# Performance work log

Measured on AMD Instinct MI355X. Metric: run time of the kernel, lower is better.

Reference implementation:

```python
import jax, jax.numpy as jnp
import numpy as np

N_WIN = 7    # n_win hardcoded in AR_Attention
TOPK = 4     # topk routing windows
HEADS = 8    # num_heads


def setup_inputs() -> dict:
    key = jax.random.key(0)
    ks = jax.random.split(key, 6)
    B, H, W, C = 4, 56, 56, 256
    s = 0.02
    x = jax.random.normal(ks[0], (B, H, W, C), jnp.float32)
    Wqkv = jax.random.normal(ks[1], (C, 3 * C), jnp.float32) * s  # Linear(dim, 3*dim) (qk_dim=dim)
    bqkv = jnp.zeros((3 * C,), jnp.float32)
    Wo = jax.random.normal(ks[2], (C, C), jnp.float32) * s        # output projection Linear(dim, dim)
    bo = jnp.zeros((C,), jnp.float32)
    lepe_w = jax.random.normal(ks[3], (5, 5, 1, C), jnp.float32) * s  # 5x5 depthwise conv (side_dwconv=5)
    lepe_b = jnp.zeros((C,), jnp.float32)
    return {"x": x, "Wqkv": Wqkv, "bqkv": bqkv, "Wo": Wo, "bo": bo,
            "lepe_w": lepe_w, "lepe_b": lepe_b}


def reference(x, Wqkv, bqkv, Wo, bo, lepe_w, lepe_b):
    B, H, W, C = x.shape
    nw = N_WIN
    h, w = H // nw, W // nw           # region size (8x8)
    p2 = nw * nw                      # number of regions (49)
    hd = C // HEADS                   # head dim
    scale = float(C) ** -0.5          # qk_scale = qk_dim ** -0.5 (qk_dim = dim)

    # region partition: [B,H,W,C] -> [B,p2,h,w,C]
    xr = x.reshape(B, nw, h, nw, w, C).transpose(0, 1, 3, 2, 4, 5).reshape(B, p2, h, w, C)

    qkv = xr @ Wqkv + bqkv            # [B,p2,h,w,3C]
    q, kv = qkv[..., :C], qkv[..., C:]

    q_pix = q.reshape(B, p2, h * w, C)
    kv_pix = kv.reshape(B, p2, h * w, 2 * C)   # kv_downsample_mode='identity'

    # region-level queries/keys via per-window mean pooling
    q_win = q.mean((2, 3))                     # [B,p2,C]
    k_win = kv[..., :C].mean((2, 3))           # [B,p2,C]

    # LEPE: 5x5 depthwise conv on v over the full image grid
    v_img = kv[..., C:].reshape(B, nw, nw, h, w, C).transpose(0, 1, 3, 2, 4, 5).reshape(B, H, W, C)
    lepe = jax.lax.conv_general_dilated(
        v_img, lepe_w, (1, 1), 'SAME',
        dimension_numbers=('NHWC', 'HWIO', 'NHWC'),
        feature_group_count=C) + lepe_b

    # top-k window routing (param_routing=False, hard routing, mul_weight='none')
    r_logit = jnp.einsum('bpc,bqc->bpq', q_win * scale, k_win)  # [B,p2,p2]
    _, r_idx = jax.lax.top_k(r_logit, TOPK)                     # [B,p2,TOPK]

    # gather selected kv windows: [B,p2,TOPK,h*w,2C]
    kv_sel = jax.vmap(lambda kvp, i: kvp[i])(kv_pix, r_idx)

    k_sel = kv_sel[..., :C].reshape(B, p2, TOPK * h * w, HEADS, hd)
    v_sel = kv_sel[..., C:].reshape(B, p2, TOPK * h * w, HEADS, hd)
    qh = q_pix.reshape(B, p2, h * w, HEADS, hd)

    attn = jnp.einsum('bpqnd,bpknd->bpnqk', qh * scale, k_sel)  # [B,p2,heads,hw,TOPK*hw]
    attn = jax.nn.softmax(attn, axis=-1)
    out = jnp.einsum('bpnqk,bpknd->bpqnd', attn, v_sel).reshape(B, p2, h, w, C)

    # windows back to image grid
    out = out.reshape(B, nw, nw, h, w, C).transpose(0, 1, 3, 2, 4, 5).reshape(B, H, W, C)
    out = out + lepe
    return out @ Wo + bo
```

## Files before the change

kernel.cpp:

```cpp
#include <hip/hip_runtime.h>
#include <hip/hip_bf16.h>

#define NPIX 12544

typedef short bf16x8 __attribute__((ext_vector_type(8)));
typedef short bf16x4 __attribute__((ext_vector_type(4)));
typedef float f32x4  __attribute__((ext_vector_type(4)));

__device__ __forceinline__ float bf2f(unsigned short u) {
    unsigned int x = ((unsigned int)u) << 16;
    float f; __builtin_memcpy(&f, &x, sizeof(f)); return f;
}
__device__ __forceinline__ unsigned short f2bf(float f) {
    __hip_bfloat16 h = __float2bfloat16(f);
    unsigned short u; __builtin_memcpy(&u, &h, 2); return u;
}
__device__ __forceinline__ void load_lds16(const unsigned short* g, unsigned short* l) {
    __builtin_amdgcn_global_load_lds(
        (const __attribute__((address_space(1))) unsigned int*)g,
        (__attribute__((address_space(3))) unsigned int*)l,
        16, 0, 0);
}
__device__ __forceinline__ unsigned ldsoff(const void* p) {
    return (unsigned)(unsigned long long)(const __attribute__((address_space(3))) char*)p;
}
template<int OFF>
__device__ __forceinline__ bf16x4 tr16(unsigned addr) {
    bf16x4 d;
    asm volatile("ds_read_b64_tr_b16 %0, %1 offset:%c2"
                 : "=v"(d) : "v"(addr), "i"(OFF));
    return d;
}

__global__ __launch_bounds__(256) void k_prep(
    const float* __restrict__ X, unsigned short* __restrict__ Xb,
    float* __restrict__ xmean,
    const float* __restrict__ Wqkv, const float* __restrict__ Wo,
    unsigned short* __restrict__ Wtq, unsigned short* __restrict__ Wto)
{
    __shared__ __align__(16) unsigned char sm[64 * 65 * 4];
    const int t = threadIdx.x;
    const int blk = blockIdx.x;
    if (blk < 392) {
        float* part = (float*)sm;
        const int w = blk >> 1, hc = blk & 1;
        const int b = w / 49, p = w % 49;
        const int wi = p / 7, wj = p % 7;
        const int ch0 = hc * 128;
        const int ps = t >> 5, cg = t & 31;
        float4 s = {0.f, 0.f, 0.f, 0.f};
        #pragma unroll
        for (int i = 0; i < 8; i++) {
            int pp = ps * 8 + i;
            int y = wi * 8 + (pp >> 3), x = wj * 8 + (pp & 7);
            int idx = (((b * 56) + y) * 56 + x) * 256 + ch0 + cg * 4;
            float4 v = *reinterpret_cast<const float4*>(X + idx);
            s.x += v.x; s.y += v.y; s.z += v.z; s.w += v.w;
            ushort4 o = { f2bf(v.x), f2bf(v.y), f2bf(v.z), f2bf(v.w) };
            *reinterpret_cast<ushort4*>(Xb + idx) = o;
        }
        *reinterpret_cast<float4*>(part + t * 4) = *reinterpret_cast<float4*>(&s);
        __syncthreads();
        if (t < 32) {
            float4 m = {0.f, 0.f, 0.f, 0.f};
            #pragma unroll
            for (int ps2 = 0; ps2 < 8; ps2++) {
                float4 v = *reinterpret_cast<float4*>(part + (ps2 * 32 + t) * 4);
                m.x += v.x; m.y += v.y; m.z += v.z; m.w += v.w;
            }
            m.x *= (1.f / 64.f); m.y *= (1.f / 64.f);
            m.z *= (1.f / 64.f); m.w *= (1.f / 64.f);
            *reinterpret_cast<float4*>(xmean + w * 256 + ch0 + t * 4) = m;
        }
    } else {
        float* tile = (float*)sm;
        int tb = blk - 392;
        const float* Wsrc; unsigned short* Wdst; int N, kt, nt;
        if (tb < 48) { Wsrc = Wqkv; Wdst = Wtq; N = 768; kt = tb / 12; nt = tb % 12; }
        else { tb -= 48; Wsrc = Wo; Wdst = Wto; N = 256; kt = tb / 4; nt = tb % 4; }
        const int k0 = kt * 64, n0 = nt * 64;
        const int r0 = t >> 6, c = t & 63;
        #pragma unroll
        for (int i = 0; i < 16; i++) {
            int r = i * 4 + r0;
            tile[r * 65 + c] = Wsrc[(size_t)(k0 + r) * N + n0 + c];
        }
        __syncthreads();
        #pragma unroll
        for (int i = 0; i < 16; i++) {
            int n = i * 4 + r0;
            Wdst[(size_t)(n0 + n) * 256 + k0 + c] = f2bf(tile[c * 65 + n]);
        }
    }
}

__global__ __launch_bounds__(256) void k_main1(
    const unsigned short* __restrict__ A,
    const unsigned short* __restrict__ Bt,
    const float* __restrict__ bias,
    unsigned short* __restrict__ O,
    const float* __restrict__ xmean,
    const float* __restrict__ Wqkv,
    float* __restrict__ qwin, float* __restrict__ kwin)
{
    __shared__ __align__(16) unsigned char sm1[32768];
    const int t = threadIdx.x;
    const int blk = blockIdx.x;
    if (blk < 588) {
        unsigned short* As = (unsigned short*)sm1;
        unsigned short* Bs = (unsigned short*)(sm1 + 16384);
        const int m0 = (blk % 98) * 128, n0 = (blk / 98) * 128;
        const int wave = t >> 6, lane = t & 63, quad = lane >> 4, lo = lane & 15;
        const int wm = wave & 1, wn = wave >> 1;
        const int sr = wave * 16 + (lane >> 2);
        const int sc = lane & 3;
        f32x4 acc[4][4];
        #pragma unroll
        for (int i = 0; i < 4; i++)
            #pragma unroll
            for (int j = 0; j < 4; j++) acc[i][j] = (f32x4){0.f, 0.f, 0.f, 0.f};

        auto stage = [&](int it) {
            int kt = it * 32;
            unsigned short* Ad = As + (it & 1) * 4096;
            unsigned short* Bd = Bs + (it & 1) * 4096;
            #pragma unroll
            for (int j = 0; j < 2; j++) {
                int row = j * 64 + sr;
                int e = sc ^ ((row >> 1) & 3);
                load_lds16(A  + (size_t)(m0 + row) * 256 + kt + e * 8, &Ad[row * 32 + sc * 8]);
                load_lds16(Bt + (size_t)(n0 + row) * 256 + kt + e * 8, &Bd[row * 32 + sc * 8]);
            }
        };
        stage(0);
        for (int it = 0; it < 8; ++it) {
            if (it < 7) {
                stage(it + 1);
                asm volatile("s_waitcnt vmcnt(4)" ::: "memory");
            } else {
                asm volatile("s_waitcnt vmcnt(0)" ::: "memory");
            }
            __builtin_amdgcn_s_barrier();
            const unsigned short* Ac = As + (it & 1) * 4096;
            const unsigned short* Bc = Bs + (it & 1) * 4096;
            bf16x8 af[4], bfr[4];
            #pragma unroll
            for (int mt = 0; mt < 4; mt++) {
                int row = wm * 64 + mt * 16 + lo;
                int c = quad ^ ((row >> 1) & 3);
                af[mt] = *reinterpret_cast<const bf16x8*>(&Ac[row * 32 + c * 8]);
            }
            #pragma unroll
            for (int nt = 0; nt < 4; nt++) {
                int col = wn * 64 + nt * 16 + lo;
                int c = quad ^ ((col >> 1) & 3);
                bfr[nt] = *reinterpret_cast<const bf16x8*>(&Bc[col * 32 + c * 8]);
            }
            #pragma unroll
            for (int mt = 0; mt < 4; mt++)
                #pragma unroll
                for (int nt = 0; nt < 4; nt++)
                    acc[mt][nt] = __builtin_amdgcn_mfma_f32_16x16x32_bf16(
                        af[mt], bfr[nt], acc[mt][nt], 0, 0, 0);
            __builtin_amdgcn_s_barrier();
        }
        float bv[4];
        #pragma unroll
        for (int nt = 0; nt < 4; nt++) bv[nt] = bias[n0 + wn * 64 + nt * 16 + lo];
        #pragma unroll
        for (int mt = 0; mt < 4; mt++)
            #pragma unroll
            for (int nt = 0; nt < 4; nt++) {
                int n = n0 + wn * 64 + nt * 16 + lo;
                #pragma unroll
                for (int r = 0; r < 4; r++) {
                    int m = m0 + wm * 64 + mt * 16 + quad * 4 + r;
                    O[m * 768 + n] = f2bf(acc[mt][nt][r] + bv[nt]);
                }
            }
    } else {
        float* xs = (float*)sm1;
        const int u = blk - 588;
        const int bp = u % 196;
        const int half = u / 196;
        const int c = t;
        xs[c] = xmean[bp * 256 + c];
        __syncthreads();
        const int col = half * 256 + c;
        float a = 0.f;
        for (int k = 0; k < 256; k++) a += xs[k] * Wqkv[k * 768 + col];
        float* outp = half ? kwin : qwin;
        outp[bp * 256 + c] = a + bias[col];
    }
}

__global__ __launch_bounds__(256) void k_main2(
    const float* __restrict__ qwin, const float* __restrict__ kwin,
    int* __restrict__ ridx)
{
    __shared__ __align__(16) unsigned char sm2[1024];
    const int t = threadIdx.x;
    const int blk = blockIdx.x;
    float* part = (float*)sm2;
    float* lg   = (float*)(sm2 + 49 * 4 * 4);
    const int b = blk / 49, p = blk % 49;
    if (t < 196) {
        int d = t >> 2, pr = t & 3;
        const float* qp = &qwin[(b * 49 + p) * 256];
        const float* kp = &kwin[(b * 49 + d) * 256];
        float a = 0.f;
        for (int ch = pr * 64; ch < pr * 64 + 64; ch++) a += qp[ch] * kp[ch];
        part[d * 4 + pr] = a;
    }
    __syncthreads();
    if (t < 49) lg[t] = part[t * 4 + 0] + part[t * 4 + 1] + part[t * 4 + 2] + part[t * 4 + 3];
    __syncthreads();
    if (t == 0) {
        unsigned long long used = 0ull;
        for (int sel = 0; sel < 4; sel++) {
            float best = -1e30f; int bi = 0;
            for (int qq = 0; qq < 49; qq++)
                if (!((used >> qq) & 1ull) && lg[qq] > best) { best = lg[qq]; bi = qq; }
            used |= (1ull << bi);
            ridx[blk * 4 + sel] = bi;
        }
    }
}

__global__ __launch_bounds__(256) void k_attn(
    const unsigned short* __restrict__ QKV,
    const int* __restrict__ ridx,
    const float* __restrict__ lw, const float* __restrict__ lb,
    unsigned short* __restrict__ Osum)
{
    __shared__ __align__(16) unsigned char smem[40064];
    unsigned short* Vs  = (unsigned short*)smem;
    unsigned short* Ks  = (unsigned short*)(smem + 16384);
    unsigned short* PST = (unsigned short*)(smem + 32768);
    float* lws          = (float*)(smem + 36864);

    const int p = blockIdx.x, head = blockIdx.y, b = blockIdx.z;
    const int t = threadIdx.x;
    const int wi = p / 7, wj = p % 7;
    const int wave = t >> 6, lane = t & 63, quad = lane >> 4, lo = lane & 15;
    const int pix4 = t >> 2, c4 = t & 3;

    const int q  = wave * 16 + lo;
    const int qy = wi * 8 + (q >> 3), qx = wj * 8 + (q & 7);

    bf16x8 af = *reinterpret_cast<const bf16x8*>(
        QKV + (size_t)(((b * 56) + qy) * 56 + qx) * 768 + head * 32 + quad * 8);

    if (t < 200) {
        int tap = t >> 3, ci = (t & 7) * 4;
        *reinterpret_cast<float4*>(&lws[tap * 32 + ci]) =
            *reinterpret_cast<const float4*>(lw + tap * 256 + head * 32 + ci);
    }
    {
        const int4 rs = *reinterpret_cast<const int4*>(&ridx[(b * 49 + p) * 4]);
        const int sels[4] = { rs.x, rs.y, rs.z, rs.w };
        #pragma unroll
        for (int pass = 0; pass < 4; pass++) {
            int sel = sels[pass];
            int si = sel / 7, sj = sel % 7;
            int y = si * 8 + (pix4 >> 3), x = sj * 8 + (pix4 & 7);
            const unsigned short* base = QKV + (((b * 56) + y) * 56 + x) * 768 + 256 + head * 32;
            bf16x8 kv = *reinterpret_cast<const bf16x8*>(base + c4 * 8);
            bf16x8 vv = *reinterpret_cast<const bf16x8*>(base + 256 + c4 * 8);
            int krow = pass * 64 + pix4;
            *reinterpret_cast<bf16x8*>(&Ks[krow * 32 + c4 * 8]) = kv;
            *reinterpret_cast<bf16x8*>(
                &Vs[(krow >> 2) * 128 + (c4 >> 1) * 64 + (krow & 3) * 16 + (c4 & 1) * 8]) = vv;
        }
    }
    __syncthreads();

    float lep[8];
    {
        float4 b0 = *reinterpret_cast<const float4*>(lb + head * 32 + quad * 8);
        float4 b1 = *reinterpret_cast<const float4*>(lb + head * 32 + quad * 8 + 4);
        lep[0] = b0.x; lep[1] = b0.y; lep[2] = b0.z; lep[3] = b0.w;
        lep[4] = b1.x; lep[5] = b1.y; lep[6] = b1.z; lep[7] = b1.w;
        #pragma unroll
        for (int ky = 0; ky < 5; ky++) {
            int yy = qy + ky - 2;
            int yc = min(max(yy, 0), 55);
            bool yin = (yy >= 0) & (yy < 56);
            #pragma unroll
            for (int kx = 0; kx < 5; kx++) {
                int xx = qx + kx - 2;
                int xc = min(max(xx, 0), 55);
                float mf = (yin & (xx >= 0) & (xx < 56)) ? 1.f : 0.f;
                bf16x8 v = *reinterpret_cast<const bf16x8*>(
                    QKV + (size_t)(((b * 56) + yc) * 56 + xc) * 768 + 512 + head * 32 + quad * 8);
                const float* wrow = &lws[(ky * 5 + kx) * 32 + quad * 8];
                float4 w0 = *reinterpret_cast<const float4*>(wrow);
                float4 w1 = *reinterpret_cast<const float4*>(wrow + 4);
                lep[0] += bf2f((unsigned short)v[0]) * w0.x * mf;
                lep[1] += bf2f((unsigned short)v[1]) * w0.y * mf;
                lep[2] += bf2f((unsigned short)v[2]) * w0.z * mf;
                lep[3] += bf2f((unsigned short)v[3]) * w0.w * mf;
                lep[4] += bf2f((unsigned short)v[4]) * w1.x * mf;
                lep[5] += bf2f((unsigned short)v[5]) * w1.y * mf;
                lep[6] += bf2f((unsigned short)v[6]) * w1.z * mf;
                lep[7] += bf2f((unsigned short)v[7]) * w1.w * mf;
            }
        }
    }

    const f32x4 z = (f32x4){0.f, 0.f, 0.f, 0.f};

    float M[4] = {-1e30f, -1e30f, -1e30f, -1e30f};
    #pragma unroll 4
    for (int nt = 0; nt < 16; nt++) {
        bf16x8 bfr = *reinterpret_cast<const bf16x8*>(&Ks[(nt * 16 + lo) * 32 + quad * 8]);
        f32x4 s = __builtin_amdgcn_mfma_f32_16x16x32_bf16(af, bfr, z, 0, 0, 0);
        #pragma unroll
        for (int r = 0; r < 4; r++) M[r] = fmaxf(M[r], s[r] * 0.0625f);
    }
    #pragma unroll
    for (int d = 1; d < 16; d <<= 1)
        #pragma unroll
        for (int r = 0; r < 4; r++) M[r] = fmaxf(M[r], __shfl_xor(M[r], d));

    unsigned short* myP = PST + wave * 512;
    const unsigned pbase = ldsoff(myP) + quad * 256 + lo * 8;
    const unsigned vbase = ldsoff(Vs)  + quad * 512 + lo * 8;
    float l[4] = {0.f, 0.f, 0.f, 0.f};
    f32x4 o0 = z, o1 = z;
    for (int c = 0; c < 8; c++) {
        bf16x8 k0 = *reinterpret_cast<const bf16x8*>(&Ks[((2 * c) * 16 + lo) * 32 + quad * 8]);
        bf16x8 k1 = *reinterpret_cast<const bf16x8*>(&Ks[((2 * c + 1) * 16 + lo) * 32 + quad * 8]);
        f32x4 s0 = __builtin_amdgcn_mfma_f32_16x16x32_bf16(af, k0, z, 0, 0, 0);
        f32x4 s1 = __builtin_amdgcn_mfma_f32_16x16x32_bf16(af, k1, z, 0, 0, 0);
        float e0[4], e1[4];
        #pragma unroll
        for (int r = 0; r < 4; r++) {
            e0[r] = __expf(s0[r] * 0.0625f - M[r]);
            e1[r] = __expf(s1[r] * 0.0625f - M[r]);
            l[r] += e0[r] + e1[r];
        }
        ushort4 p0 = { f2bf(e0[0]), f2bf(e0[1]), f2bf(e0[2]), f2bf(e0[3]) };
        ushort4 p1 = { f2bf(e1[0]), f2bf(e1[1]), f2bf(e1[2]), f2bf(e1[3]) };
        *reinterpret_cast<ushort4*>(&myP[lo * 16 + quad * 4]) = p0;
        *reinterpret_cast<ushort4*>(&myP[(16 + lo) * 16 + quad * 4]) = p1;
        asm volatile("s_waitcnt lgkmcnt(0)" ::: "memory");
        __builtin_amdgcn_sched_barrier(0);

        const unsigned vb = vbase + c * 2048;
        bf16x4 ra0  = tr16<0>(pbase);
        bf16x4 ra1  = tr16<128>(pbase);
        bf16x4 rw00 = tr16<0>(vb);
        bf16x4 rw01 = tr16<256>(vb);
        bf16x4 rw10 = tr16<128>(vb);
        bf16x4 rw11 = tr16<384>(vb);
        asm volatile("s_waitcnt lgkmcnt(0)" ::: "memory");
        __builtin_amdgcn_sched_barrier(0);
        bf16x8 pa, vb0, vb1;
        #pragma unroll
        for (int j = 0; j < 4; j++) {
            pa[j]  = ra0[j];  pa[4 + j]  = ra1[j];
            vb0[j] = rw00[j]; vb0[4 + j] = rw01[j];
            vb1[j] = rw10[j]; vb1[4 + j] = rw11[j];
        }
        o0 = __builtin_amdgcn_mfma_f32_16x16x32_bf16(pa, vb0, o0, 0, 0, 0);
        o1 = __builtin_amdgcn_mfma_f32_16x16x32_bf16(pa, vb1, o1, 0, 0, 0);
    }
    #pragma unroll
    for (int d = 1; d < 16; d <<= 1)
        #pragma unroll
        for (int r = 0; r < 4; r++) l[r] += __shfl_xor(l[r], d);

    {
        float i0 = 1.f / l[0], i1 = 1.f / l[1], i2 = 1.f / l[2], i3 = 1.f / l[3];
        ushort4 p0 = { f2bf(o0[0] * i0), f2bf(o0[1] * i1),
                       f2bf(o0[2] * i2), f2bf(o0[3] * i3) };
        ushort4 p1 = { f2bf(o1[0] * i0), f2bf(o1[1] * i1),
                       f2bf(o1[2] * i2), f2bf(o1[3] * i3) };
        *reinterpret_cast<ushort4*>(&myP[lo * 16 + quad * 4]) = p0;
        *reinterpret_cast<ushort4*>(&myP[(16 + lo) * 16 + quad * 4]) = p1;
    }
    const unsigned oaddr = ldsoff(myP) + quad * 256 + lo * 8;
    asm volatile("s_waitcnt lgkmcnt(0)" ::: "memory");
    __builtin_amdgcn_sched_barrier(0);
    bf16x4 e0 = tr16<0>(oaddr);
    bf16x4 e1 = tr16<128>(oaddr);
    asm volatile("s_waitcnt lgkmcnt(0)" ::: "memory");
    __builtin_amdgcn_sched_barrier(0);
    {
        size_t gbase = (size_t)(((b * 56) + qy) * 56 + qx) * 256 + head * 32 + quad * 8;
        bf16x8 oo;
        #pragma unroll
        for (int j = 0; j < 4; j++) {
            oo[j]     = (short)f2bf(bf2f((unsigned short)e0[j]) + lep[j]);
            oo[4 + j] = (short)f2bf(bf2f((unsigned short)e1[j]) + lep[4 + j]);
        }
        *reinterpret_cast<bf16x8*>(Osum + gbase) = oo;
    }
}

__global__ __launch_bounds__(256) void k_proj(
    const unsigned short* __restrict__ A,
    const unsigned short* __restrict__ Bt,
    const float* __restrict__ bias,
    float* __restrict__ O)
{
    __shared__ __align__(16) unsigned short As[2 * 128 * 32];
    __shared__ __align__(16) unsigned short Bs[2 * 64 * 32];
    const int t = threadIdx.x;
    const int m0 = blockIdx.x * 128, n0 = blockIdx.y * 64;
    const int wave = t >> 6, lane = t & 63, quad = lane >> 4, lo = lane & 15;
    const int sr = wave * 16 + (lane >> 2);
    const int sc = lane & 3;
    f32x4 acc[2][4];
    #pragma unroll
    for (int i = 0; i < 2; i++)
        #pragma unroll
        for (int j = 0; j < 4; j++) acc[i][j] = (f32x4){0.f, 0.f, 0.f, 0.f};

    auto stage = [&](int it) {
        int kt = it * 32;
        unsigned short* Ad = As + (it & 1) * 4096;
        unsigned short* Bd = Bs + (it & 1) * 2048;
        #pragma unroll
        for (int j = 0; j < 2; j++) {
            int row = j * 64 + sr;
            int e = sc ^ ((row >> 1) & 3);
            load_lds16(A + (size_t)(m0 + row) * 256 + kt + e * 8, &Ad[row * 32 + sc * 8]);
        }
        {
            int e = sc ^ ((sr >> 1) & 3);
            load_lds16(Bt + (size_t)(n0 + sr) * 256 + kt + e * 8, &Bd[sr * 32 + sc * 8]);
        }
    };
    stage(0);
    for (int it = 0; it < 8; ++it) {
        if (it < 7) {
            stage(it + 1);
            asm volatile("s_waitcnt vmcnt(3)" ::: "memory");
        } else {
            asm volatile("s_waitcnt vmcnt(0)" ::: "memory");
        }
        __builtin_amdgcn_s_barrier();
        const unsigned short* Ac = As + (it & 1) * 4096;
        const unsigned short* Bc = Bs + (it & 1) * 2048;
        bf16x8 af[2], bfr[4];
        #pragma unroll
        for (int mt = 0; mt < 2; mt++) {
            int row = wave * 32 + mt * 16 + lo;
            int c = quad ^ ((row >> 1) & 3);
            af[mt] = *reinterpret_cast<const bf16x8*>(&Ac[row * 32 + c * 8]);
        }
        #pragma unroll
        for (int nt = 0; nt < 4; nt++) {
            int col = nt * 16 + lo;
            int c = quad ^ ((col >> 1) & 3);
            bfr[nt] = *reinterpret_cast<const bf16x8*>(&Bc[col * 32 + c * 8]);
        }
        #pragma unroll
        for (int mt = 0; mt < 2; mt++)
            #pragma unroll
            for (int nt = 0; nt < 4; nt++)
                acc[mt][nt] = __builtin_amdgcn_mfma_f32_16x16x32_bf16(
                    af[mt], bfr[nt], acc[mt][nt], 0, 0, 0);
        __builtin_amdgcn_s_barrier();
    }
    float bv[4];
    #pragma unroll
    for (int nt = 0; nt < 4; nt++) bv[nt] = bias[n0 + nt * 16 + lo];
    #pragma unroll
    for (int mt = 0; mt < 2; mt++)
        #pragma unroll
        for (int nt = 0; nt < 4; nt++) {
            int n = n0 + nt * 16 + lo;
            #pragma unroll
            for (int r = 0; r < 4; r++) {
                int m = m0 + wave * 32 + mt * 16 + quad * 4 + r;
                O[m * 256 + n] = acc[mt][nt][r] + bv[nt];
            }
        }
}

extern "C" void kernel_launch(void* const* d_in, const int* in_sizes, int n_in,
                              void* d_out, int out_size, void* d_ws, size_t ws_size,
                              hipStream_t stream)
{
    const float* x    = (const float*)d_in[0];
    const float* Wqkv = (const float*)d_in[1];
    const float* bqkv = (const float*)d_in[2];
    const float* Wo   = (const float*)d_in[3];
    const float* bo   = (const float*)d_in[4];
    const float* lw   = (const float*)d_in[5];
    const float* lb   = (const float*)d_in[6];
    float* out = (float*)d_out;

    char* ws = (char*)d_ws;
    size_t off = 0;
    unsigned short* qkv   = (unsigned short*)(ws + off); off += (size_t)NPIX * 768 * 2;
    unsigned short* xb    = (unsigned short*)(ws + off); off += (size_t)NPIX * 256 * 2;
    unsigned short* Wtq   = (unsigned short*)(ws + off); off += 768 * 256 * 2;
    unsigned short* Wto   = (unsigned short*)(ws + off); off += 256 * 256 * 2;
    unsigned short* Osum  = (unsigned short*)(ws + off); off += (size_t)NPIX * 256 * 2;
    float* xmean = (float*)(ws + off); off += 196 * 256 * 4;
    float* qwin  = (float*)(ws + off); off += 196 * 256 * 4;
    float* kwin  = (float*)(ws + off); off += 196 * 256 * 4;
    int*   ridx  = (int*)(ws + off);   off += 196 * 4 * 4;

    k_prep <<<dim3(456),      256, 0, stream>>>(x, xb, xmean, Wqkv, Wo, Wtq, Wto);
    k_main1<<<dim3(980),      256, 0, stream>>>(xb, Wtq, bqkv, qkv, xmean, Wqkv, qwin, kwin);
    k_main2<<<dim3(196),      256, 0, stream>>>(qwin, kwin, ridx);
    k_attn <<<dim3(49, 8, 4), 256, 0, stream>>>(qkv, ridx, lw, lb, Osum);
    k_proj <<<dim3(98, 4),    256, 0, stream>>>(Osum, Wto, bo, out);
}
```

Baseline: 181.2 us.

## Move LEPE depthwise conv out of attention into routing kernel as separate blocks

The 5x5 depthwise LEPE conv is taken out of the attention kernel and computed by extra blocks appended to the routing kernel. Those blocks write a bf16 LEPE buffer, and the attention kernel reads it back at the end. This is meant to shorten the attention kernel's critical path and register and LDS use, and to run the conv alongside the small routing work. The cost is an extra global write and read of a pixel-by-channel bf16 buffer, plus one more rounding of the LEPE term to bf16.

```diff
diff --git a/kernel.cpp b/kernel.cpp
--- a/kernel.cpp
+++ b/kernel.cpp
@@ -196,48 +196,99 @@
 
 __global__ __launch_bounds__(256) void k_main2(
     const float* __restrict__ qwin, const float* __restrict__ kwin,
-    int* __restrict__ ridx)
+    int* __restrict__ ridx,
+    const unsigned short* __restrict__ QKV,
+    const float* __restrict__ lw, const float* __restrict__ lb,
+    unsigned short* __restrict__ Olepe)
 {
-    __shared__ __align__(16) unsigned char sm2[1024];
+    __shared__ __align__(16) unsigned char sm2[25600];
     const int t = threadIdx.x;
     const int blk = blockIdx.x;
-    float* part = (float*)sm2;
-    float* lg   = (float*)(sm2 + 49 * 4 * 4);
-    const int b = blk / 49, p = blk % 49;
-    if (t < 196) {
-        int d = t >> 2, pr = t & 3;
-        const float* qp = &qwin[(b * 49 + p) * 256];
-        const float* kp = &kwin[(b * 49 + d) * 256];
-        float a = 0.f;
-        for (int ch = pr * 64; ch < pr * 64 + 64; ch++) a += qp[ch] * kp[ch];
-        part[d * 4 + pr] = a;
-    }
-    __syncthreads();
-    if (t < 49) lg[t] = part[t * 4 + 0] + part[t * 4 + 1] + part[t * 4 + 2] + part[t * 4 + 3];
-    __syncthreads();
-    if (t == 0) {
-        unsigned long long used = 0ull;
-        for (int sel = 0; sel < 4; sel++) {
-            float best = -1e30f; int bi = 0;
-            for (int qq = 0; qq < 49; qq++)
-                if (!((used >> qq) & 1ull) && lg[qq] > best) { best = lg[qq]; bi = qq; }
-            used |= (1ull << bi);
-            ridx[blk * 4 + sel] = bi;
-        }
+    if (blk < 196) {
+        float* part = (float*)sm2;
+        float* lg   = (float*)(sm2 + 49 * 4 * 4);
+        const int b = blk / 49, p = blk % 49;
+        if (t < 196) {
+            int d = t >> 2, pr = t & 3;
+            const float* qp = &qwin[(b * 49 + p) * 256];
+            const float* kp = &kwin[(b * 49 + d) * 256];
+            float a = 0.f;
+            for (int ch = pr * 64; ch < pr * 64 + 64; ch++) a += qp[ch] * kp[ch];
+            part[d * 4 + pr] = a;
+        }
+        __syncthreads();
+        if (t < 49) lg[t] = part[t * 4 + 0] + part[t * 4 + 1] + part[t * 4 + 2] + part[t * 4 + 3];
+        __syncthreads();
+        if (t == 0) {
+            unsigned long long used = 0ull;
+            for (int sel = 0; sel < 4; sel++) {
+                float best = -1e30f; int bi = 0;
+                for (int qq = 0; qq < 49; qq++)
+                    if (!((used >> qq) & 1ull) && lg[qq] > best) { best = lg[qq]; bi = qq; }
+                used |= (1ull << bi);
+                ridx[blk * 4 + sel] = bi;
+            }
+        }
+    } else {
+        float* lws = (float*)sm2;
+        #pragma unroll
+        for (int i = 0; i < 25; i++) lws[i * 256 + t] = lw[i * 256 + t];
+
+        const int pl = t & 7;
+        const int cg = t >> 3;
+        const int c0 = cg * 8;
+        const int gid = (blk - 196) * 8 + pl;
+        const int b = gid / 3136, rem = gid % 3136;
+        const int y = rem / 56, x = rem % 56;
+        __syncthreads();
+
+        float acc[8];
+        {
+            float4 b0 = *reinterpret_cast<const float4*>(lb + c0);
+            float4 b1 = *reinterpret_cast<const float4*>(lb + c0 + 4);
+            acc[0] = b0.x; acc[1] = b0.y; acc[2] = b0.z; acc[3] = b0.w;
+            acc[4] = b1.x; acc[5] = b1.y; acc[6] = b1.z; acc[7] = b1.w;
+        }
+        #pragma unroll
+        for (int ky = 0; ky < 5; ky++) {
+            int yy = y + ky - 2;
+            if (yy < 0 || yy >= 56) continue;
+            #pragma unroll
+            for (int kx = 0; kx < 5; kx++) {
+                int xx = x + kx - 2;
+                if (xx < 0 || xx >= 56) continue;
+                bf16x8 v = *reinterpret_cast<const bf16x8*>(
+                    QKV + (((b * 56) + yy) * 56 + xx) * 768 + 512 + c0);
+                const float* wrow = &lws[(ky * 5 + kx) * 256 + c0];
+                float4 w0 = *reinterpret_cast<const float4*>(wrow);
+                float4 w1 = *reinterpret_cast<const float4*>(wrow + 4);
+                acc[0] += bf2f((unsigned short)v[0]) * w0.x;
+                acc[1] += bf2f((unsigned short)v[1]) * w0.y;
+                acc[2] += bf2f((unsigned short)v[2]) * w0.z;
+                acc[3] += bf2f((unsigned short)v[3]) * w0.w;
+                acc[4] += bf2f((unsigned short)v[4]) * w1.x;
+                acc[5] += bf2f((unsigned short)v[5]) * w1.y;
+                acc[6] += bf2f((unsigned short)v[6]) * w1.z;
+                acc[7] += bf2f((unsigned short)v[7]) * w1.w;
+            }
+        }
+        bf16x8 o;
+        #pragma unroll
+        for (int j = 0; j < 8; j++) o[j] = (short)f2bf(acc[j]);
+        *reinterpret_cast<bf16x8*>(Olepe + (size_t)gid * 256 + c0) = o;
     }
 }
 
 __global__ __launch_bounds__(256) void k_attn(
     const unsigned short* __restrict__ QKV,
     const int* __restrict__ ridx,
-    const float* __restrict__ lw, const float* __restrict__ lb,
+    const unsigned short* __restrict__ Olepe,
     unsigned short* __restrict__ Osum)
 {
-    __shared__ __align__(16) unsigned char smem[40064];
+    __shared__ __align__(16) unsigned char smem[36864];
     unsigned short* Vs  = (unsigned short*)smem;
     unsigned short* Ks  = (unsigned short*)(smem + 16384);
     unsigned short* PST = (unsigned short*)(smem + 32768);
-    float* lws          = (float*)(smem + 36864);
 
     const int p = blockIdx.x, head = blockIdx.y, b = blockIdx.z;
     const int t = threadIdx.x;
@@ -251,11 +302,6 @@
     bf16x8 af = *reinterpret_cast<const bf16x8*>(
         QKV + (size_t)(((b * 56) + qy) * 56 + qx) * 768 + head * 32 + quad * 8);
 
-    if (t < 200) {
-        int tap = t >> 3, ci = (t & 7) * 4;
-        *reinterpret_cast<float4*>(&lws[tap * 32 + ci]) =
-            *reinterpret_cast<const float4*>(lw + tap * 256 + head * 32 + ci);
-    }
     {
         const int4 rs = *reinterpret_cast<const int4*>(&ridx[(b * 49 + p) * 4]);
         const int sels[4] = { rs.x, rs.y, rs.z, rs.w };
@@ -275,39 +321,6 @@
     }
     __syncthreads();
 
-    float lep[8];
-    {
-        float4 b0 = *reinterpret_cast<const float4*>(lb + head * 32 + quad * 8);
-        float4 b1 = *reinterpret_cast<const float4*>(lb + head * 32 + quad * 8 + 4);
-        lep[0] = b0.x; lep[1] = b0.y; lep[2] = b0.z; lep[3] = b0.w;
-        lep[4] = b1.x; lep[5] = b1.y; lep[6] = b1.z; lep[7] = b1.w;
-        #pragma unroll
-        for (int ky = 0; ky < 5; ky++) {
-            int yy = qy + ky - 2;
-            int yc = min(max(yy, 0), 55);
-            bool yin = (yy >= 0) & (yy < 56);
-            #pragma unroll
-            for (int kx = 0; kx < 5; kx++) {
-                int xx = qx + kx - 2;
-                int xc = min(max(xx, 0), 55);
-                float mf = (yin & (xx >= 0) & (xx < 56)) ? 1.f : 0.f;
-                bf16x8 v = *reinterpret_cast<const bf16x8*>(
-                    QKV + (size_t)(((b * 56) + yc) * 56 + xc) * 768 + 512 + head * 32 + quad * 8);
-                const float* wrow = &lws[(ky * 5 + kx) * 32 + quad * 8];
-                float4 w0 = *reinterpret_cast<const float4*>(wrow);
-                float4 w1 = *reinterpret_cast<const float4*>(wrow + 4);
-                lep[0] += bf2f((unsigned short)v[0]) * w0.x * mf;
-                lep[1] += bf2f((unsigned short)v[1]) * w0.y * mf;
-                lep[2] += bf2f((unsigned short)v[2]) * w0.z * mf;
-                lep[3] += bf2f((unsigned short)v[3]) * w0.w * mf;
-                lep[4] += bf2f((unsigned short)v[4]) * w1.x * mf;
-                lep[5] += bf2f((unsigned short)v[5]) * w1.y * mf;
-                lep[6] += bf2f((unsigned short)v[6]) * w1.z * mf;
-                lep[7] += bf2f((unsigned short)v[7]) * w1.w * mf;
-            }
-        }
-    }
-
     const f32x4 z = (f32x4){0.f, 0.f, 0.f, 0.f};
 
     float M[4] = {-1e30f, -1e30f, -1e30f, -1e30f};
@@ -389,11 +402,12 @@
     __builtin_amdgcn_sched_barrier(0);
     {
         size_t gbase = (size_t)(((b * 56) + qy) * 56 + qx) * 256 + head * 32 + quad * 8;
+        bf16x8 lp = *reinterpret_cast<const bf16x8*>(Olepe + gbase);
         bf16x8 oo;
         #pragma unroll
         for (int j = 0; j < 4; j++) {
-            oo[j]     = (short)f2bf(bf2f((unsigned short)e0[j]) + lep[j]);
-            oo[4 + j] = (short)f2bf(bf2f((unsigned short)e1[j]) + lep[4 + j]);
+            oo[j]     = (short)f2bf(bf2f((unsigned short)e0[j]) + bf2f((unsigned short)lp[j]));
+            oo[4 + j] = (short)f2bf(bf2f((unsigned short)e1[j]) + bf2f((unsigned short)lp[4 + j]));
         }
         *reinterpret_cast<bf16x8*>(Osum + gbase) = oo;
     }
@@ -501,6 +515,7 @@
     unsigned short* Wtq   = (unsigned short*)(ws + off); off += 768 * 256 * 2;
     unsigned short* Wto   = (unsigned short*)(ws + off); off += 256 * 256 * 2;
     unsigned short* Osum  = (unsigned short*)(ws + off); off += (size_t)NPIX * 256 * 2;
+    unsigned short* Olepe = (unsigned short*)(ws + off); off += (size_t)NPIX * 256 * 2;
     float* xmean = (float*)(ws + off); off += 196 * 256 * 4;
     float* qwin  = (float*)(ws + off); off += 196 * 256 * 4;
     float* kwin  = (float*)(ws + off); off += 196 * 256 * 4;
@@ -508,7 +523,7 @@
 
     k_prep <<<dim3(456),      256, 0, stream>>>(x, xb, xmean, Wqkv, Wo, Wtq, Wto);
     k_main1<<<dim3(980),      256, 0, stream>>>(xb, Wtq, bqkv, qkv, xmean, Wqkv, qwin, kwin);
-    k_main2<<<dim3(196),      256, 0, stream>>>(qwin, kwin, ridx);
-    k_attn <<<dim3(49, 8, 4), 256, 0, stream>>>(qkv, ridx, lw, lb, Osum);
+    k_main2<<<dim3(1764),     256, 0, stream>>>(qwin, kwin, ridx, qkv, lw, lb, Olepe);
+    k_attn <<<dim3(49, 8, 4), 256, 0, stream>>>(qkv, ridx, Olepe, Osum);
     k_proj <<<dim3(98, 4),    256, 0, stream>>>(Osum, Wto, bo, out);
 }
```

Result: faster. 151.7 us (-16.3%).
